# Optimization experiments

Measured on AMD Instinct MI355X. Metric: run time of the kernel, lower is better.

The kernel has to match this reference:

```python
import jax, jax.numpy as jnp
import numpy as np

B, N = 16, 4096
N_IN, E_OUT = 128, 128          # inpt_dim[1], outp_dim[0]
OUT_N = 128                     # outp_dim[1]
G_DIM, CTXT_DIM = 64, 64
NODE_IN = E_OUT + N_IN          # 256, pre_ln size
CTXT_IN = G_DIM + CTXT_DIM      # 128
HID_F, HID_A = 256, 128
N_HEADS = 4
HEAD_DIM = OUT_N // N_HEADS     # 32
LN_EPS = 1e-5


def _init_w(key, fan_in, fan_out):
    return jax.random.normal(key, (fan_in, fan_out), jnp.float32) / np.float32(np.sqrt(fan_in))


def setup_inputs() -> dict:
    key = jax.random.key(0)
    ks = jax.random.split(key, 10)
    nodes = jax.random.normal(ks[0], (B, N, N_IN), jnp.float32)
    pooled_edges = jax.random.normal(ks[1], (B, N, E_OUT), jnp.float32)
    # variable-length graphs: valid prefix per graph (at least half the nodes)
    lengths = jax.random.randint(ks[2], (B,), N // 2, N + 1)
    mask = jnp.arange(N)[None, :] < lengths[:, None]
    globs = jax.random.normal(ks[3], (B, G_DIM), jnp.float32)
    ctxt = jax.random.normal(ks[4], (B, CTXT_DIM), jnp.float32)
    return {
        "nodes": nodes,
        "pooled_edges": pooled_edges,
        "mask": mask,
        "globs": globs,
        "ctxt": ctxt,
        "ln_g": jnp.ones((NODE_IN,), jnp.float32),
        "ln_b": jnp.zeros((NODE_IN,), jnp.float32),
        "feat_w1": _init_w(ks[5], NODE_IN + CTXT_IN, HID_F),
        "feat_b1": jnp.zeros((HID_F,), jnp.float32),
        "feat_w2": _init_w(ks[6], HID_F, OUT_N),
        "feat_b2": jnp.zeros((OUT_N,), jnp.float32),
        "attn_w1": _init_w(ks[7], NODE_IN + CTXT_IN, HID_A),
        "attn_b1": jnp.zeros((HID_A,), jnp.float32),
        "attn_w2": _init_w(ks[8], HID_A, N_HEADS),
        "attn_b2": jnp.zeros((N_HEADS,), jnp.float32),
    }


def _mlp(x, w1, b1, w2, b2):
    # DenseNetwork: one hidden block with LeakyReLU ("lrlu"), linear output
    h = jax.nn.leaky_relu(x @ w1 + b1)
    return h @ w2 + b2


def reference(nodes, pooled_edges, mask, globs, ctxt, ln_g, ln_b,
              feat_w1, feat_b1, feat_w2, feat_b2,
              attn_w1, attn_b1, attn_w2, attn_b2):
    # nodes = cat([graph.nodes, pooled_edges]) -> pre-LayerNorm
    x = jnp.concatenate([nodes, pooled_edges], axis=-1)           # [B,N,256]
    mu = jnp.mean(x, axis=-1, keepdims=True)
    var = jnp.var(x, axis=-1, keepdims=True)
    x = (x - mu) * jax.lax.rsqrt(var + LN_EPS) * ln_g + ln_b

    # high-level context broadcast to every node
    hl = jnp.concatenate([globs, ctxt], axis=-1)                   # [B,128]
    hl = jnp.broadcast_to(hl[:, None, :], (x.shape[0], x.shape[1], hl.shape[-1]))
    xin = jnp.concatenate([x, hl], axis=-1)                        # [B,N,384]

    # attention net with -inf padding, softmax over node axis (dim=-2)
    logits = _mlp(xin, attn_w1, attn_b1, attn_w2, attn_b2)          # [B,N,H]
    logits = jnp.where(mask[..., None], logits, -jnp.inf)
    w = jax.nn.softmax(logits, axis=1) / np.float32(np.sqrt(OUT_N))
    w = jnp.where(mask[..., None], w, 0.0)

    # feature net with 0 padding + residual (same_size)
    feats = _mlp(xin, feat_w1, feat_b1, feat_w2, feat_b2)           # [B,N,128]
    feats = jnp.where(mask[..., None], feats, 0.0)
    new_nodes = feats + nodes

    # expand per-head weights across head_dim, flatten, weighted node pooling
    w_full = jnp.repeat(w, HEAD_DIM, axis=-1)                       # [B,N,128]
    pooled = jnp.sum(new_nodes * w_full, axis=1)                    # [B,128]
    return (new_nodes, pooled)
```

## Files before the change

kernel.cpp:

```cpp
#include <hip/hip_runtime.h>
#include <stdint.h>

typedef unsigned short u16;
typedef unsigned char  u8;
typedef unsigned int   u32;
typedef __attribute__((ext_vector_type(8))) short bf16x8;
typedef __attribute__((ext_vector_type(4))) float f32x4;

static __device__ __forceinline__ float bf2f(u32 u) {
    union { u32 i; float f; } x; x.i = u << 16; return x.f;
}
static __device__ __forceinline__ u16 f2bf(float f) {
    union { u32 i; float f; } x; x.f = f;
    return (u16)((x.i + 0x7fffu + ((x.i >> 16) & 1u)) >> 16);
}
static __device__ __forceinline__ u32 packbf(float a, float b) {
    return (u32)f2bf(a) | ((u32)f2bf(b) << 16);
}
static __device__ __forceinline__ float ldf(const void* p, int i, int isf32) {
    return isf32 ? ((const float*)p)[i] : bf2f(((const u16*)p)[i]);
}
static __device__ __forceinline__ bool mvalid(const void* mask, int g, int mi32) {
    return mi32 ? (((const int*)mask)[g] != 0) : (((const u8*)mask)[g] != 0);
}

#define NTOT 65536
#define SXLD 264
#define SHLD 136
#define PVLD 144

__global__ __launch_bounds__(256) void k0_prep(
    const void* __restrict__ feat_w1, const void* __restrict__ attn_w1,
    const void* __restrict__ feat_b1, const void* __restrict__ attn_b1,
    const void* __restrict__ feat_w2, const void* __restrict__ attn_w2,
    const void* __restrict__ globs, const void* __restrict__ ctxt,
    const void* __restrict__ ln_g,
    u16* __restrict__ W1t, u16* __restrict__ W2t, u16* __restrict__ aw2t,
    float* __restrict__ hlc)
{
    __shared__ u16 tile[64][66];
    __shared__ float hl[128];
    const int isf32 = (((const u32*)ln_g)[0] == 0x3F800000u);
    const int bid = blockIdx.x;
    const int t = threadIdx.x;

    if (bid < 24) {
        int jt = bid >> 2, kt = bid & 3;
        int j0 = jt * 64, k0 = kt * 64;
        int jj = t & 63, kq = t >> 6;
#pragma unroll
        for (int r = 0; r < 16; r++) {
            int kk = r * 4 + kq;
            int j = j0 + jj;
            float v = (j < 256) ? ldf(feat_w1, (k0 + kk) * 256 + j, isf32)
                                : ldf(attn_w1, (k0 + kk) * 128 + (j - 256), isf32);
            tile[kk][jj] = f2bf(v);
        }
        __syncthreads();
        int kk2 = t & 63, jq = t >> 6;
#pragma unroll
        for (int r = 0; r < 16; r++) {
            int jj2 = r * 4 + jq;
            W1t[(size_t)(j0 + jj2) * 256 + k0 + kk2] = tile[kk2][jj2];
        }
    } else if (bid < 32) {
        int id2 = bid - 24;
        int ct2 = id2 >> 2, kt = id2 & 3;
        int c0 = ct2 * 64, k0 = kt * 64;
        int cc = t & 63, kq = t >> 6;
#pragma unroll
        for (int r = 0; r < 16; r++) {
            int kk = r * 4 + kq;
            tile[kk][cc] = f2bf(ldf(feat_w2, (k0 + kk) * 128 + c0 + cc, isf32));
        }
        __syncthreads();
        int kk2 = t & 63, cq = t >> 6;
#pragma unroll
        for (int r = 0; r < 16; r++) {
            int cc2 = r * 4 + cq;
            W2t[(size_t)(c0 + cc2) * 256 + k0 + kk2] = tile[kk2][cc2];
        }
    } else if (bid == 32) {
#pragma unroll
        for (int i = 0; i < 8; i++) {
            int e = i * 256 + t;
            int n = e >> 7, k = e & 127;
            aw2t[e] = (n < 4) ? f2bf(ldf(attn_w2, k * 4 + n, isf32)) : (u16)0;
        }
    } else {
        int b = bid - 33;
        if (t < 64)       hl[t] = ldf(globs, b * 64 + t, isf32);
        else if (t < 128) hl[t] = ldf(ctxt, b * 64 + (t - 64), isf32);
        __syncthreads();
        {
            float s = ldf(feat_b1, t, isf32);
#pragma unroll 8
            for (int c = 0; c < 128; c++)
                s += hl[c] * ldf(feat_w1, (256 + c) * 256 + t, isf32);
            hlc[b * 384 + t] = s;
        }
        if (t < 128) {
            float s = ldf(attn_b1, t, isf32);
#pragma unroll 8
            for (int c = 0; c < 128; c++)
                s += hl[c] * ldf(attn_w1, (256 + c) * 128 + t, isf32);
            hlc[b * 384 + 256 + t] = s;
        }
    }
}

__global__ __launch_bounds__(512, 4) void k_mega(
    const void* __restrict__ nodes, const void* __restrict__ edges,
    const void* __restrict__ ln_g, const void* __restrict__ ln_b,
    const u16* __restrict__ W1t, const u16* __restrict__ W2t,
    const u16* __restrict__ aw2t, const float* __restrict__ hlc,
    const void* __restrict__ attn_b2, const void* __restrict__ feat_b2,
    const void* __restrict__ mask,
    float* __restrict__ pv, void* __restrict__ outp)
{
    __shared__ __align__(16) u16 sX[64 * SXLD];
    __shared__ __align__(16) u16 sH[64 * SHLD];
    __shared__ float sG[256], sBt[256];
    __shared__ float sL[64][4];
    const int t = threadIdx.x;
    const int g0 = blockIdx.x * 64;
    const int b = g0 >> 12;
    const int isf32 = (((const u32*)ln_g)[0] == 0x3F800000u);
    const int mi32  = (((const u32*)mask)[0] == 1u);

    if (t < 256) { sG[t] = ldf(ln_g, t, isf32); sBt[t] = ldf(ln_b, t, isf32); }
    __syncthreads();

    {
        const int r = t >> 3, q8 = t & 7;
        u32 pk[16];
#pragma unroll
        for (int j = 0; j < 4; j++) {
            int c = q8 + j * 8;
            if (isf32) {
                const float* src = (c < 16)
                    ? ((const float*)nodes + (size_t)(g0 + r) * 128 + c * 8)
                    : ((const float*)edges + (size_t)(g0 + r) * 128 + (c - 16) * 8);
                float4 v0 = ((const float4*)src)[0];
                float4 v1 = ((const float4*)src)[1];
                pk[4 * j]     = packbf(v0.x, v0.y);
                pk[4 * j + 1] = packbf(v0.z, v0.w);
                pk[4 * j + 2] = packbf(v1.x, v1.y);
                pk[4 * j + 3] = packbf(v1.z, v1.w);
            } else {
                const u16* src = (c < 16)
                    ? ((const u16*)nodes + (size_t)(g0 + r) * 128 + c * 8)
                    : ((const u16*)edges + (size_t)(g0 + r) * 128 + (c - 16) * 8);
                uint4 v = ((const uint4*)src)[0];
                pk[4 * j] = v.x; pk[4 * j + 1] = v.y;
                pk[4 * j + 2] = v.z; pk[4 * j + 3] = v.w;
            }
        }
        float s = 0.f, q = 0.f;
#pragma unroll
        for (int i = 0; i < 16; i++) {
            float lo = bf2f(pk[i] & 0xffffu), hi = bf2f(pk[i] >> 16);
            s += lo + hi; q += lo * lo + hi * hi;
        }
        s += __shfl_xor(s, 1, 64); s += __shfl_xor(s, 2, 64); s += __shfl_xor(s, 4, 64);
        q += __shfl_xor(q, 1, 64); q += __shfl_xor(q, 2, 64); q += __shfl_xor(q, 4, 64);
        float mu = s * (1.f / 256.f);
        float var = q * (1.f / 256.f) - mu * mu;
        float rs = rsqrtf(var + 1e-5f);
#pragma unroll
        for (int j = 0; j < 4; j++) {
            int c = q8 + j * 8;
            u32 ow[4];
#pragma unroll
            for (int k2 = 0; k2 < 4; k2++) {
                int col = c * 8 + k2 * 2;
                u32 w2 = pk[4 * j + k2];
                float y0 = (bf2f(w2 & 0xffffu) - mu) * rs * sG[col]     + sBt[col];
                float y1 = (bf2f(w2 >> 16)     - mu) * rs * sG[col + 1] + sBt[col + 1];
                ow[k2] = packbf(y0, y1);
            }
            *(uint4*)&sX[r * SXLD + c * 8] = make_uint4(ow[0], ow[1], ow[2], ow[3]);
        }
    }
    __syncthreads();

    const int w = t >> 6, l = t & 63;
    const int lr = l & 15, lq = l >> 4;
    const int cb = w * 16;
    const float ab2 = (lr < 4) ? ldf(attn_b2, lr, isf32) : 0.f;
    const float fb2 = ldf(feat_b2, cb + lr, isf32);
    float* pvb = pv + (size_t)blockIdx.x * PVLD;

    f32x4 acc2[4];
#pragma unroll
    for (int rt = 0; rt < 4; rt++) acc2[rt] = (f32x4){0.f, 0.f, 0.f, 0.f};

    float nv[4][4];
    bool  mrow[4][4];

    const int order[3] = {2, 0, 1};
#pragma unroll
    for (int oi = 0; oi < 3; oi++) {
        const int nt = order[oi];
        const float hbv = hlc[b * 384 + nt * 128 + cb + lr];

        f32x4 acc1[4];
#pragma unroll
        for (int rt = 0; rt < 4; rt++) acc1[rt] = (f32x4){0.f, 0.f, 0.f, 0.f};

        const u16* Wp = W1t + (size_t)(nt * 128 + cb + lr) * 256;
#pragma unroll
        for (int kh = 0; kh < 2; kh++) {
            bf16x8 bW[4];
#pragma unroll
            for (int kk = 0; kk < 4; kk++)
                bW[kk] = *(const bf16x8*)(Wp + (kh * 4 + kk) * 32 + lq * 8);
#pragma unroll
            for (int kk = 0; kk < 4; kk++) {
                bf16x8 aF[4];
#pragma unroll
                for (int rt = 0; rt < 4; rt++)
                    aF[rt] = *(const bf16x8*)&sX[(rt * 16 + lr) * SXLD + ((kh * 4 + kk) * 4 + lq) * 8];
#pragma unroll
                for (int rt = 0; rt < 4; rt++)
                    acc1[rt] = __builtin_amdgcn_mfma_f32_16x16x32_bf16(aF[rt], bW[kk], acc1[rt], 0, 0, 0);
            }
        }

        __syncthreads();
#pragma unroll
        for (int rt = 0; rt < 4; rt++)
#pragma unroll
            for (int reg = 0; reg < 4; reg++) {
                int row = rt * 16 + lq * 4 + reg;
                float hv = acc1[rt][reg] + hbv;
                hv = (hv >= 0.f) ? hv : 0.01f * hv;
                sH[row * SHLD + cb + lr] = f2bf(hv);
            }

        if (oi == 1 && w < 4) {
            const int row = l;
            const bool vld = mvalid(mask, g0 + row, mi32);
            float lg = sL[row][w];
            float x = vld ? lg : -1e30f;
#pragma unroll
            for (int o = 1; o < 64; o <<= 1) x = fmaxf(x, __shfl_xor(x, o, 64));
            float e = vld ? expf(lg - x) : 0.f;
            sL[row][w] = e;
            float sgm = e;
#pragma unroll
            for (int o = 1; o < 64; o <<= 1) sgm += __shfl_xor(sgm, o, 64);
            if (l == 0) { pvb[128 + w] = sgm; pvb[132 + w] = x; }
        }
        __syncthreads();

        if (nt == 2) {
            if (w < 4) {
                f32x4 accL = (f32x4){0.f, 0.f, 0.f, 0.f};
#pragma unroll
                for (int kk = 0; kk < 4; kk++) {
                    bf16x8 aF = *(const bf16x8*)&sH[(w * 16 + lr) * SHLD + (kk * 4 + lq) * 8];
                    bf16x8 bF = *(const bf16x8*)(aw2t + lr * 128 + kk * 32 + lq * 8);
                    accL = __builtin_amdgcn_mfma_f32_16x16x32_bf16(aF, bF, accL, 0, 0, 0);
                }
                if (lr < 4) {
#pragma unroll
                    for (int reg = 0; reg < 4; reg++)
                        sL[w * 16 + lq * 4 + reg][lr] = accL[reg] + ab2;
                }
            }
        } else {
            if (oi == 2) {
#pragma unroll
                for (int rt = 0; rt < 4; rt++)
#pragma unroll
                    for (int reg = 0; reg < 4; reg++) {
                        int row = rt * 16 + lq * 4 + reg;
                        mrow[rt][reg] = mvalid(mask, g0 + row, mi32);
                        nv[rt][reg] = ldf(nodes, (g0 + row) * 128 + cb + lr, isf32);
                    }
            }
            const u16* W2p = W2t + (size_t)(cb + lr) * 256 + nt * 128;
            bf16x8 bW2[4];
#pragma unroll
            for (int kk = 0; kk < 4; kk++)
                bW2[kk] = *(const bf16x8*)(W2p + kk * 32 + lq * 8);
#pragma unroll
            for (int kk = 0; kk < 4; kk++) {
                bf16x8 aF[4];
#pragma unroll
                for (int rt = 0; rt < 4; rt++)
                    aF[rt] = *(const bf16x8*)&sH[(rt * 16 + lr) * SHLD + (kk * 4 + lq) * 8];
#pragma unroll
                for (int rt = 0; rt < 4; rt++)
                    acc2[rt] = __builtin_amdgcn_mfma_f32_16x16x32_bf16(aF[rt], bW2[kk], acc2[rt], 0, 0, 0);
            }
        }
    }

    float pc = 0.f;
#pragma unroll
    for (int rt = 0; rt < 4; rt++)
#pragma unroll
        for (int reg = 0; reg < 4; reg++) {
            int row = rt * 16 + lq * 4 + reg;
            int g = g0 + row;
            float v = acc2[rt][reg] + fb2;
            v = mrow[rt][reg] ? v : 0.f;
            v += nv[rt][reg];
            size_t idx = (size_t)g * 128 + cb + lr;
            if (isf32) ((float*)outp)[idx] = v;
            else       ((u16*)outp)[idx] = f2bf(v);
            pc += sL[row][w >> 1] * v;
        }
    pc += __shfl_xor(pc, 16, 64); pc += __shfl_xor(pc, 32, 64);
    if (lq == 0) pvb[cb + lr] = pc;
}

__global__ __launch_bounds__(256) void k_final(
    const float* __restrict__ pv, const void* __restrict__ ln_g,
    void* __restrict__ outbase)
{
    __shared__ float sm[64], ss[64], se[64];
    __shared__ float sZ;
    __shared__ float part[8][32];
    const int blk = blockIdx.x;
    const int b = blk >> 2, q = blk & 3;
    const int t = threadIdx.x;
    const int isf32 = (((const u32*)ln_g)[0] == 0x3F800000u);
    const float* pvb = pv + (size_t)b * 64 * PVLD;

    if (t < 128) {
        int rec = t >> 1, j = t & 1;
        float x = pvb[(size_t)rec * PVLD + 128 + j * 4 + q];
        if (j == 0) ss[rec] = x;
        else        sm[rec] = x;
    }
    __syncthreads();

    if (t < 64) {
        float m = sm[t];
#pragma unroll
        for (int o = 1; o < 64; o <<= 1) m = fmaxf(m, __shfl_xor(m, o, 64));
        float e = expf(sm[t] - m);
        se[t] = e;
        float z = e * ss[t];
#pragma unroll
        for (int o = 1; o < 64; o <<= 1) z += __shfl_xor(z, o, 64);
        if (t == 0) sZ = z;
    }
    __syncthreads();

    {
        const int ci = t & 31, rg = t >> 5;
        const int c = q * 32 + ci;
        float acc = 0.f;
#pragma unroll
        for (int j = 0; j < 8; j++) {
            int rec = rg * 8 + j;
            acc += se[rec] * pvb[(size_t)rec * PVLD + c];
        }
        part[rg][ci] = acc;
    }
    __syncthreads();
    if (t < 32) {
        float s = 0.f;
#pragma unroll
        for (int r = 0; r < 8; r++) s += part[r][t];
        float p = s * (0.08838834764831845f / sZ);
        size_t off = (size_t)NTOT * 128 + (size_t)b * 128 + q * 32 + t;
        if (isf32) ((float*)outbase)[off] = p;
        else       ((u16*)outbase)[off] = f2bf(p);
    }
}

extern "C" void kernel_launch(void* const* d_in, const int* in_sizes, int n_in,
                              void* d_out, int out_size, void* d_ws, size_t ws_size,
                              hipStream_t stream)
{
    const void* nodes   = d_in[0];
    const void* edges   = d_in[1];
    const void* mask    = d_in[2];
    const void* globs   = d_in[3];
    const void* ctxt    = d_in[4];
    const void* ln_g    = d_in[5];
    const void* ln_b    = d_in[6];
    const void* feat_w1 = d_in[7];
    const void* feat_b1 = d_in[8];
    const void* feat_w2 = d_in[9];
    const void* feat_b2 = d_in[10];
    const void* attn_w1 = d_in[11];
    const void* attn_b1 = d_in[12];
    const void* attn_w2 = d_in[13];
    const void* attn_b2 = d_in[14];

    char* ws = (char*)d_ws;
    u16*   W1t    = (u16*)ws;   ws += (size_t)384 * 256 * 2;
    u16*   W2t    = (u16*)ws;   ws += (size_t)128 * 256 * 2;
    u16*   aw2t   = (u16*)ws;   ws += (size_t)16 * 128 * 2;
    float* hlc    = (float*)ws; ws += (size_t)16 * 384 * 4;
    float* pv     = (float*)ws; ws += (size_t)1024 * PVLD * 4;

    k0_prep <<<dim3(49),   dim3(256), 0, stream>>>(feat_w1, attn_w1, feat_b1, attn_b1,
                                                   feat_w2, attn_w2, globs, ctxt, ln_g,
                                                   W1t, W2t, aw2t, hlc);
    k_mega  <<<dim3(1024), dim3(512), 0, stream>>>(nodes, edges, ln_g, ln_b, W1t, W2t,
                                                   aw2t, hlc, attn_b2, feat_b2, mask,
                                                   pv, d_out);
    k_final <<<dim3(64),   dim3(256), 0, stream>>>(pv, ln_g, d_out);
}
```

Before: 196.4 us.

## Retile mega kernel warps to 32x32 output tiles for operand reuse

Each of the 8 warps now computes a 32-row by 32-column tile instead of all 64 rows by 16 columns. Every A fragment read from shared memory now feeds two MFMAs instead of one, which cuts LDS traffic per MFMA. It also means each warp loads twice as many weight fragments from global memory, raises register pressure, and needs a shared-memory reduction with an extra barrier to combine the two row halves of the pooled partial sums.

```diff
diff --git a/kernel.cpp b/kernel.cpp
--- a/kernel.cpp
+++ b/kernel.cpp
@@ -122,6 +122,7 @@
     __shared__ __align__(16) u16 sH[64 * SHLD];
     __shared__ float sG[256], sBt[256];
     __shared__ float sL[64][4];
+    __shared__ float pcol[2][128];
     const int t = threadIdx.x;
     const int g0 = blockIdx.x * 64;
     const int b = g0 >> 12;
@@ -186,57 +187,76 @@
 
     const int w = t >> 6, l = t & 63;
     const int lr = l & 15, lq = l >> 4;
-    const int cb = w * 16;
+    const int rh = w >> 2;
+    const int cq = w & 3;
+    const int cb = cq * 32;
+    const int r0 = rh * 32;
     const float ab2 = (lr < 4) ? ldf(attn_b2, lr, isf32) : 0.f;
-    const float fb2 = ldf(feat_b2, cb + lr, isf32);
+    const float fb2_0 = ldf(feat_b2, cb + lr, isf32);
+    const float fb2_1 = ldf(feat_b2, cb + 16 + lr, isf32);
     float* pvb = pv + (size_t)blockIdx.x * PVLD;
 
-    f32x4 acc2[4];
-#pragma unroll
-    for (int rt = 0; rt < 4; rt++) acc2[rt] = (f32x4){0.f, 0.f, 0.f, 0.f};
-
-    float nv[4][4];
-    bool  mrow[4][4];
+    f32x4 acc2[2][2];
+#pragma unroll
+    for (int rt = 0; rt < 2; rt++)
+#pragma unroll
+        for (int ct = 0; ct < 2; ct++) acc2[rt][ct] = (f32x4){0.f, 0.f, 0.f, 0.f};
+
+    float nv[2][2][4];
+    bool  mrow[2][4];
 
     const int order[3] = {2, 0, 1};
 #pragma unroll
     for (int oi = 0; oi < 3; oi++) {
         const int nt = order[oi];
-        const float hbv = hlc[b * 384 + nt * 128 + cb + lr];
-
-        f32x4 acc1[4];
-#pragma unroll
-        for (int rt = 0; rt < 4; rt++) acc1[rt] = (f32x4){0.f, 0.f, 0.f, 0.f};
+
+        float hbv[2];
+#pragma unroll
+        for (int ct = 0; ct < 2; ct++)
+            hbv[ct] = hlc[b * 384 + nt * 128 + cb + ct * 16 + lr];
+
+        f32x4 acc1[2][2];
+#pragma unroll
+        for (int rt = 0; rt < 2; rt++)
+#pragma unroll
+            for (int ct = 0; ct < 2; ct++) acc1[rt][ct] = (f32x4){0.f, 0.f, 0.f, 0.f};
 
         const u16* Wp = W1t + (size_t)(nt * 128 + cb + lr) * 256;
 #pragma unroll
         for (int kh = 0; kh < 2; kh++) {
-            bf16x8 bW[4];
+            bf16x8 bW[4][2];
 #pragma unroll
             for (int kk = 0; kk < 4; kk++)
-                bW[kk] = *(const bf16x8*)(Wp + (kh * 4 + kk) * 32 + lq * 8);
+#pragma unroll
+                for (int ct = 0; ct < 2; ct++)
+                    bW[kk][ct] = *(const bf16x8*)(Wp + ct * 16 * 256 + (kh * 4 + kk) * 32 + lq * 8);
 #pragma unroll
             for (int kk = 0; kk < 4; kk++) {
-                bf16x8 aF[4];
-#pragma unroll
-                for (int rt = 0; rt < 4; rt++)
-                    aF[rt] = *(const bf16x8*)&sX[(rt * 16 + lr) * SXLD + ((kh * 4 + kk) * 4 + lq) * 8];
-#pragma unroll
-                for (int rt = 0; rt < 4; rt++)
-                    acc1[rt] = __builtin_amdgcn_mfma_f32_16x16x32_bf16(aF[rt], bW[kk], acc1[rt], 0, 0, 0);
+                bf16x8 aF[2];
+#pragma unroll
+                for (int rt = 0; rt < 2; rt++)
+                    aF[rt] = *(const bf16x8*)&sX[(r0 + rt * 16 + lr) * SXLD + ((kh * 4 + kk) * 4 + lq) * 8];
+#pragma unroll
+                for (int rt = 0; rt < 2; rt++)
+#pragma unroll
+                    for (int ct = 0; ct < 2; ct++)
+                        acc1[rt][ct] = __builtin_amdgcn_mfma_f32_16x16x32_bf16(aF[rt], bW[kk][ct], acc1[rt][ct], 0, 0, 0);
             }
         }
 
         __syncthreads();
 #pragma unroll
-        for (int rt = 0; rt < 4; rt++)
-#pragma unroll
-            for (int reg = 0; reg < 4; reg++) {
-                int row = rt * 16 + lq * 4 + reg;
-                float hv = acc1[rt][reg] + hbv;
-                hv = (hv >= 0.f) ? hv : 0.01f * hv;
-                sH[row * SHLD + cb + lr] = f2bf(hv);
-            }
+        for (int rt = 0; rt < 2; rt++)
+#pragma unroll
+            for (int ct = 0; ct < 2; ct++)
+#pragma unroll
+                for (int reg = 0; reg < 4; reg++) {
+                    int row = r0 + rt * 16 + lq * 4 + reg;
+                    int col = cb + ct * 16 + lr;
+                    float hv = acc1[rt][ct][reg] + hbv[ct];
+                    hv = (hv >= 0.f) ? hv : 0.01f * hv;
+                    sH[row * SHLD + col] = f2bf(hv);
+                }
 
         if (oi == 1 && w < 4) {
             const int row = l;
@@ -272,49 +292,66 @@
         } else {
             if (oi == 2) {
 #pragma unroll
-                for (int rt = 0; rt < 4; rt++)
+                for (int rt = 0; rt < 2; rt++)
 #pragma unroll
                     for (int reg = 0; reg < 4; reg++) {
-                        int row = rt * 16 + lq * 4 + reg;
+                        int row = r0 + rt * 16 + lq * 4 + reg;
                         mrow[rt][reg] = mvalid(mask, g0 + row, mi32);
-                        nv[rt][reg] = ldf(nodes, (g0 + row) * 128 + cb + lr, isf32);
+#pragma unroll
+                        for (int ct = 0; ct < 2; ct++)
+                            nv[rt][ct][reg] = ldf(nodes,
+                                (g0 + row) * 128 + cb + ct * 16 + lr, isf32);
                     }
             }
             const u16* W2p = W2t + (size_t)(cb + lr) * 256 + nt * 128;
-            bf16x8 bW2[4];
+            bf16x8 bW2[4][2];
 #pragma unroll
             for (int kk = 0; kk < 4; kk++)
-                bW2[kk] = *(const bf16x8*)(W2p + kk * 32 + lq * 8);
+#pragma unroll
+                for (int ct = 0; ct < 2; ct++)
+                    bW2[kk][ct] = *(const bf16x8*)(W2p + ct * 16 * 256 + kk * 32 + lq * 8);
 #pragma unroll
             for (int kk = 0; kk < 4; kk++) {
-                bf16x8 aF[4];
-#pragma unroll
-                for (int rt = 0; rt < 4; rt++)
-                    aF[rt] = *(const bf16x8*)&sH[(rt * 16 + lr) * SHLD + (kk * 4 + lq) * 8];
-#pragma unroll
-                for (int rt = 0; rt < 4; rt++)
-                    acc2[rt] = __builtin_amdgcn_mfma_f32_16x16x32_bf16(aF[rt], bW2[kk], acc2[rt], 0, 0, 0);
-            }
-        }
-    }
-
-    float pc = 0.f;
-#pragma unroll
-    for (int rt = 0; rt < 4; rt++)
-#pragma unroll
-        for (int reg = 0; reg < 4; reg++) {
-            int row = rt * 16 + lq * 4 + reg;
-            int g = g0 + row;
-            float v = acc2[rt][reg] + fb2;
-            v = mrow[rt][reg] ? v : 0.f;
-            v += nv[rt][reg];
-            size_t idx = (size_t)g * 128 + cb + lr;
-            if (isf32) ((float*)outp)[idx] = v;
-            else       ((u16*)outp)[idx] = f2bf(v);
-            pc += sL[row][w >> 1] * v;
-        }
-    pc += __shfl_xor(pc, 16, 64); pc += __shfl_xor(pc, 32, 64);
-    if (lq == 0) pvb[cb + lr] = pc;
+                bf16x8 aF[2];
+#pragma unroll
+                for (int rt = 0; rt < 2; rt++)
+                    aF[rt] = *(const bf16x8*)&sH[(r0 + rt * 16 + lr) * SHLD + (kk * 4 + lq) * 8];
+#pragma unroll
+                for (int rt = 0; rt < 2; rt++)
+#pragma unroll
+                    for (int ct = 0; ct < 2; ct++)
+                        acc2[rt][ct] = __builtin_amdgcn_mfma_f32_16x16x32_bf16(aF[rt], bW2[kk][ct], acc2[rt][ct], 0, 0, 0);
+            }
+        }
+    }
+
+    float pc0 = 0.f, pc1 = 0.f;
+#pragma unroll
+    for (int rt = 0; rt < 2; rt++)
+#pragma unroll
+        for (int ct = 0; ct < 2; ct++)
+#pragma unroll
+            for (int reg = 0; reg < 4; reg++) {
+                int row = r0 + rt * 16 + lq * 4 + reg;
+                int col = cb + ct * 16 + lr;
+                int g = g0 + row;
+                float v = acc2[rt][ct][reg] + (ct ? fb2_1 : fb2_0);
+                v = mrow[rt][reg] ? v : 0.f;
+                v += nv[rt][ct][reg];
+                size_t idx = (size_t)g * 128 + col;
+                if (isf32) ((float*)outp)[idx] = v;
+                else       ((u16*)outp)[idx] = f2bf(v);
+                float e = sL[row][cq];
+                if (ct) pc1 += e * v; else pc0 += e * v;
+            }
+    pc0 += __shfl_xor(pc0, 16, 64); pc0 += __shfl_xor(pc0, 32, 64);
+    pc1 += __shfl_xor(pc1, 16, 64); pc1 += __shfl_xor(pc1, 32, 64);
+    if (lq == 0) {
+        pcol[rh][cb + lr]      = pc0;
+        pcol[rh][cb + 16 + lr] = pc1;
+    }
+    __syncthreads();
+    if (t < 128) pvb[t] = pcol[0][t] + pcol[1][t];
 }
 
 __global__ __launch_bounds__(256) void k_final(
```

Result: slower. 215.0 us (+9.5%).
